# Kernel tuning notes

Hardware: AMD Instinct MI355X
Metric: run time of the kernel (lower is better)

## Reference

```python
import jax, jax.numpy as jnp
import numpy as np

NEG_SLOPE = 0.2

def _gat_layer(x, src, dst, W, a_src, a_dst, b, n_nodes):
    # x: [N, Fin], W: [Fin, Fout], a_src/a_dst: [Fout], b: [Fout]
    h = x @ W                                  # [N, Fout]
    alpha_s = h @ a_src                        # [N]
    alpha_d = h @ a_dst                        # [N]
    e = jax.nn.leaky_relu(alpha_s[src] + alpha_d[dst], NEG_SLOPE)  # [E]
    # softmax over edges grouped by destination node
    m = jax.ops.segment_max(e, dst, num_segments=n_nodes)
    ex = jnp.exp(e - m[dst])
    denom = jax.ops.segment_sum(ex, dst, num_segments=n_nodes)
    alpha = ex / denom[dst]                    # [E]
    out = jax.ops.segment_sum(h[src] * alpha[:, None], dst, num_segments=n_nodes)
    return out + b


def setup_inputs() -> dict:
    key = jax.random.key(0)
    N, E, INP = 50000, 1600000, 128
    topo = [32, 64, 128, 128]
    OUT = 16
    ks = jax.random.split(key, 32)
    inp = {}
    inp['x'] = jax.random.normal(ks[0], (N, INP), dtype=jnp.float32)
    inp['edge_index'] = jax.random.randint(ks[1], (2, E), 0, N, dtype=jnp.int64)
    dims = [INP] + topo
    ki = 2
    for i in range(4):
        fin, fout = dims[i], dims[i + 1]
        s = 1.0 / np.sqrt(fin)
        inp[f'W{i}'] = jax.random.normal(ks[ki], (fin, fout), dtype=jnp.float32) * s; ki += 1
        inp[f'a_src{i}'] = jax.random.normal(ks[ki], (fout,), dtype=jnp.float32) * (1.0 / np.sqrt(fout)); ki += 1
        inp[f'a_dst{i}'] = jax.random.normal(ks[ki], (fout,), dtype=jnp.float32) * (1.0 / np.sqrt(fout)); ki += 1
        inp[f'b{i}'] = jnp.zeros((fout,), dtype=jnp.float32); ki += 1
    inp['fc_W'] = jax.random.normal(ks[ki], (topo[-1], OUT), dtype=jnp.float32) * (1.0 / np.sqrt(topo[-1])); ki += 1
    inp['fc_b'] = jnp.zeros((OUT,), dtype=jnp.float32)
    return inp


def reference(x, edge_index, W0, a_src0, a_dst0, b0, W1, a_src1, a_dst1, b1,
              W2, a_src2, a_dst2, b2, W3, a_src3, a_dst3, b3, fc_W, fc_b):
    n = x.shape[0]
    loops = jnp.arange(n, dtype=edge_index.dtype)
    src = jnp.concatenate([edge_index[0], loops])  # add self-loops (GATConv default)
    dst = jnp.concatenate([edge_index[1], loops])
    layers = [(W0, a_src0, a_dst0, b0), (W1, a_src1, a_dst1, b1),
              (W2, a_src2, a_dst2, b2), (W3, a_src3, a_dst3, b3)]
    for (W, a_s, a_d, b) in layers:
        x = jax.nn.relu(_gat_layer(x, src, dst, W, a_s, a_d, b, n))
    return x @ fc_W + fc_b
```

## Files before the change

kernel.cpp:

```cpp
#include <hip/hip_runtime.h>
#include <hip/hip_bf16.h>
#include <hip/hip_fp16.h>


__device__ __forceinline__ float bf2f(unsigned short w) {
    return __uint_as_float(((unsigned int)w) << 16);
}
__device__ __forceinline__ unsigned enc_f(float f) {
    unsigned u = __float_as_uint(f);
    return (u & 0x80000000u) ? ~u : (u | 0x80000000u);
}
__device__ __forceinline__ float dec_f(unsigned u) {
    unsigned v = (u & 0x80000000u) ? (u & 0x7FFFFFFFu) : ~u;
    return __uint_as_float(v);
}

#define ELL_K 96
#define NCHUNK 256

__global__ void detect_kernel(const unsigned short* __restrict__ xw,
                              const int* __restrict__ ew,
                              int* __restrict__ flags,
                              unsigned* __restrict__ maxbuf)
{
    __shared__ int cnt_sane[256];
    __shared__ int cnt_nz[256];
    const int t = threadIdx.x;
    unsigned short w = xw[2 * t];
    int e = (w >> 7) & 0xff;
    cnt_sane[t] = (e >= 110 && e <= 133) ? 1 : 0;
    cnt_nz[t] = (ew[2 * t + 1] != 0) ? 1 : 0;
    if (t < 8) maxbuf[t] = 0u;
    __syncthreads();
    if (t == 0) {
        int s = 0, nz = 0;
        for (int i = 0; i < 256; ++i) { s += cnt_sane[i]; nz += cnt_nz[i]; }
        flags[0] = (s >= 128) ? 1 : 0;
        flags[1] = (nz == 0) ? 1 : 0;
    }
}

struct ParamPtrs {
    const void* src[18];
    int n[18];
    int off[18];
};

__global__ void convert_params_kernel(ParamPtrs pp, const int* __restrict__ flags,
                                      float* __restrict__ out)
{
    const int b = blockIdx.x;
    const int n = pp.n[b];
    const float* fp = (const float*)pp.src[b];
    const unsigned short* hp = (const unsigned short*)pp.src[b];
    const int bf = flags[0];
    float* o = out + pp.off[b];
    for (int i = threadIdx.x; i < n; i += blockDim.x)
        o[i] = bf ? bf2f(hp[i]) : fp[i];
}

__global__ void wvec_kernel(const float* __restrict__ W1, const float* __restrict__ as1,
                            const float* __restrict__ ad1,
                            const float* __restrict__ W2, const float* __restrict__ as2,
                            const float* __restrict__ ad2,
                            float* __restrict__ wsd)
{
    const int l = blockIdx.x;
    const float* W  = l ? W2  : W1;
    const float* As = l ? as2 : as1;
    const float* Ad = l ? ad2 : ad1;
    const int FIN  = l ? 64 : 32;
    const int FOUT = l ? 128 : 64;
    float* ws = wsd + l * 256;
    float* wd = ws + 128;
    const int k = threadIdx.x;
    if (k < FIN) {
        float s = 0.f, d = 0.f;
        for (int j = 0; j < FOUT; ++j) {
            const float w = W[k * FOUT + j];
            s += w * As[j];
            d += w * Ad[j];
        }
        ws[k] = s;
        wd[k] = d;
    }
}

__global__ __launch_bounds__(256) void max_finalize_kernel(
    const float2* __restrict__ bm, int nb, unsigned* __restrict__ maxSD)
{
    __shared__ float sm[4][2];
    const int tx = threadIdx.x;
    float ms = -INFINITY, md = -INFINITY;
    for (int i = tx; i < nb; i += 256) {
        const float2 v = bm[i];
        ms = fmaxf(ms, v.x);
        md = fmaxf(md, v.y);
    }
    #pragma unroll
    for (int off = 32; off > 0; off >>= 1) {
        ms = fmaxf(ms, __shfl_down(ms, off, 64));
        md = fmaxf(md, __shfl_down(md, off, 64));
    }
    if ((tx & 63) == 0) { sm[tx >> 6][0] = ms; sm[tx >> 6][1] = md; }
    __syncthreads();
    if (tx == 0) {
        #pragma unroll
        for (int w = 1; w < 4; ++w) {
            ms = fmaxf(ms, sm[w][0]);
            md = fmaxf(md, sm[w][1]);
        }
        maxSD[0] = enc_f(ms);
        maxSD[1] = enc_f(md);
    }
}

template <int FIN>
__global__ __launch_bounds__(256) void alpha_matvec_kernel(
    const __half* __restrict__ x, const float* __restrict__ ws,
    const float* __restrict__ wd, float* __restrict__ as, float* __restrict__ ad,
    float2* __restrict__ blkmax, int N)
{
    constexpr int LPR = FIN / 8;
    constexpr int RPB = 256 / LPR;
    const int tx = threadIdx.x;
    const int lane = tx & 63;
    const long long row = (long long)blockIdx.x * RPB + tx / LPR;
    const int fl = (tx % LPR) * 8;
    float ss = 0.f, sd = 0.f;
    const bool valid = row < (long long)N;
    if (valid) {
        const float4 raw = *(const float4*)(x + row * FIN + fl);
        const __half2* q = (const __half2*)&raw;
        float v[8];
        float2 f;
        f = __half22float2(q[0]); v[0] = f.x; v[1] = f.y;
        f = __half22float2(q[1]); v[2] = f.x; v[3] = f.y;
        f = __half22float2(q[2]); v[4] = f.x; v[5] = f.y;
        f = __half22float2(q[3]); v[6] = f.x; v[7] = f.y;
        #pragma unroll
        for (int u = 0; u < 8; ++u) {
            const float r = fmaxf(v[u], 0.f);
            ss += r * ws[fl + u];
            sd += r * wd[fl + u];
        }
    }
    #pragma unroll
    for (int off = LPR / 2; off > 0; off >>= 1) {
        ss += __shfl_down(ss, off, 64);
        sd += __shfl_down(sd, off, 64);
    }
    const bool lead = (tx % LPR) == 0;
    if (lead && valid) { as[row] = ss; ad[row] = sd; }
    float ms = (lead && valid) ? ss : -INFINITY;
    float md = (lead && valid) ? sd : -INFINITY;
    #pragma unroll
    for (int off = 32; off > 0; off >>= 1) {
        ms = fmaxf(ms, __shfl_down(ms, off, 64));
        md = fmaxf(md, __shfl_down(md, off, 64));
    }
    if (lane == 0)
        blkmax[blockIdx.x * 4 + (tx >> 6)] = make_float2(ms, md);
}

__global__ __launch_bounds__(1024) void hist_pack_kernel(
    const int* __restrict__ e, const int* __restrict__ flags,
    unsigned* __restrict__ sd, unsigned* __restrict__ hist,
    long long E, long long Et, int chunk, int NQ)
{
    extern __shared__ unsigned hcnt[];
    const int c = blockIdx.x;
    for (int i = threadIdx.x; i < NQ; i += 1024) hcnt[i] = 0u;
    __syncthreads();
    const int f64 = flags[1];
    const long long c0 = (long long)c * chunk;
    long long c1 = c0 + chunk; if (c1 > Et) c1 = Et;
    for (long long t = c0 + threadIdx.x; t < c1; t += 1024) {
        int s, d;
        if (t >= E) { s = (int)(t - E); d = s; }
        else if (f64) { s = e[2 * t]; d = e[2 * E + 2 * t]; }
        else          { s = e[t];     d = e[E + t]; }
        sd[t] = (unsigned)s | ((unsigned)d << 16);
        atomicAdd(&hcnt[d >> 2], 1u << ((d & 3) << 3));
    }
    __syncthreads();
    unsigned* hrow = hist + (size_t)c * NQ;
    for (int i = threadIdx.x; i < NQ; i += 1024) hrow[i] = hcnt[i];
}

__global__ __launch_bounds__(256) void chunk_scan_kernel(
    const unsigned* __restrict__ hist, unsigned* __restrict__ base32,
    int* __restrict__ deg, int NQ, int N)
{
    __shared__ unsigned short sums[32][8][4];
    const int dql = threadIdx.x & 31;
    const int oct = threadIdx.x >> 5;
    const int dq  = blockIdx.x * 32 + dql;
    const int cbeg = oct * 32;

    unsigned s0 = 0, s1 = 0, s2 = 0, s3 = 0;
    if (dq < NQ) {
        const unsigned* hp = hist + (size_t)cbeg * NQ + dq;
        #pragma unroll 8
        for (int c = 0; c < 32; ++c) {
            const unsigned v = hp[(size_t)c * NQ];
            s0 += v & 0xffu;          s1 += (v >> 8) & 0xffu;
            s2 += (v >> 16) & 0xffu;  s3 += v >> 24;
        }
    }
    sums[dql][oct][0] = (unsigned short)s0;
    sums[dql][oct][1] = (unsigned short)s1;
    sums[dql][oct][2] = (unsigned short)s2;
    sums[dql][oct][3] = (unsigned short)s3;
    __syncthreads();

    unsigned r0 = 0, r1 = 0, r2 = 0, r3 = 0;
    #pragma unroll
    for (int p = 0; p < 8; ++p) {
        if (p < oct) {
            r0 += sums[dql][p][0]; r1 += sums[dql][p][1];
            r2 += sums[dql][p][2]; r3 += sums[dql][p][3];
        }
    }
    if (dq >= NQ) return;

    if (oct == 7) {
        const int d0 = dq * 4;
        const int t0 = (int)(r0 + s0), t1 = (int)(r1 + s1);
        const int t2 = (int)(r2 + s2), t3 = (int)(r3 + s3);
        if (d0 + 3 < N) {
            *(int4*)(deg + d0) = make_int4(t0, t1, t2, t3);
        } else {
            if (d0     < N) deg[d0]     = t0;
            if (d0 + 1 < N) deg[d0 + 1] = t1;
            if (d0 + 2 < N) deg[d0 + 2] = t2;
            if (d0 + 3 < N) deg[d0 + 3] = t3;
        }
    }

    unsigned run0 = r0, run1 = r1, run2 = r2, run3 = r3;
    const unsigned* hp = hist + (size_t)cbeg * NQ + dq;
    unsigned* bp = base32 + (size_t)cbeg * NQ + dq;
    for (int c = 0; c < 32; ++c) {
        const unsigned v = hp[(size_t)c * NQ];
        const unsigned o = (run0 < 255u ? run0 : 255u)
                         | ((run1 < 255u ? run1 : 255u) << 8)
                         | ((run2 < 255u ? run2 : 255u) << 16)
                         | ((run3 < 255u ? run3 : 255u) << 24);
        bp[(size_t)c * NQ] = o;
        run0 += v & 0xffu;          run1 += (v >> 8) & 0xffu;
        run2 += (v >> 16) & 0xffu;  run3 += v >> 24;
    }
}

__global__ __launch_bounds__(256) void ell_fill_kernel(
    const unsigned* __restrict__ sd, const unsigned* __restrict__ base32,
    unsigned short* __restrict__ ell16, long long Et, int chunk, int NQ, int shift)
{
    extern __shared__ unsigned cnt[];
    const int bucket = blockIdx.x & 7;
    const int c = blockIdx.x >> 3;
    const int words = (1 << shift) >> 2;
    for (int i = threadIdx.x; i < words; i += 256) cnt[i] = 0u;
    __syncthreads();
    const long long c0 = (long long)c * chunk;
    long long c1 = c0 + chunk; if (c1 > Et) c1 = Et;
    const unsigned* brow = base32 + (size_t)c * NQ;
    const int dlo = bucket << shift;
    for (long long i = c0 + threadIdx.x; i < c1; i += 256) {
        const unsigned v = sd[i];
        const int d = (int)(v >> 16);
        if ((d >> shift) != bucket) continue;
        const int dl = d - dlo;
        const unsigned sh = (unsigned)((dl & 3) << 3);
        const unsigned old = atomicAdd(&cnt[dl >> 2], 1u << sh);
        const unsigned lr = (old >> sh) & 0xffu;
        const unsigned b = (brow[d >> 2] >> ((d & 3) << 3)) & 0xffu;
        const unsigned slot = b + lr;
        if (slot < ELL_K)
            ell16[(long long)d * ELL_K + slot] = (unsigned short)(v & 0xffffu);
    }
}

struct Half4 { __half2 a, b; };

__device__ __forceinline__ void store4(float* h, long long idx, const float* a) {
    *(float4*)(h + idx) = make_float4(a[0], a[1], a[2], a[3]);
}
__device__ __forceinline__ void store4(__half* h, long long idx, const float* a) {
    Half4 v;
    v.a = __floats2half2_rn(a[0], a[1]);
    v.b = __floats2half2_rn(a[2], a[3]);
    *(Half4*)(h + idx) = v;
}

template <int FIN, int FOUT, typename OT>
__global__ __launch_bounds__(256) void gemm_alpha_kernel(
    const void* __restrict__ xv, const int* __restrict__ flags, int x_ext,
    const float* __restrict__ W, const float* __restrict__ a_src,
    const float* __restrict__ a_dst, const float* __restrict__ bias,
    OT* __restrict__ h,
    float* __restrict__ alpha_s, float* __restrict__ alpha_d,
    float2* __restrict__ blkmax, int has_alpha,
    int N, int relu_in, int has_bias)
{
    constexpr int CG = FOUT / 4;
    constexpr int RT = 256 / CG;
    constexpr int RR = 64 / RT;
    constexpr int TM = 64;
    constexpr int XP = FIN + 4;
    constexpr int Q  = FIN / 8;

    __shared__ float xs[TM * XP];
    __shared__ float red[2][TM][CG + 1];

    const int tx = threadIdx.x;
    const int cg = tx & (CG - 1);
    const int rt = tx / CG;
    const long long base = (long long)blockIdx.x * TM;

    const int xbf = x_ext ? flags[0] : 0;

    for (int idx = tx; idx < TM * Q; idx += 256) {
        const int r  = idx / Q;
        const int c8 = idx - r * Q;
        const long long grow = base + r;
        float v[8] = {0.f, 0.f, 0.f, 0.f, 0.f, 0.f, 0.f, 0.f};
        if (grow < N) {
            const long long gi = grow * FIN + 8 * c8;
            if (x_ext) {
                if (xbf) {
                    const unsigned short* xp = (const unsigned short*)xv + gi;
                    #pragma unroll
                    for (int u = 0; u < 8; ++u) v[u] = bf2f(xp[u]);
                } else {
                    const float4 f0 = *((const float4*)((const float*)xv + gi));
                    const float4 f1 = *((const float4*)((const float*)xv + gi + 4));
                    v[0] = f0.x; v[1] = f0.y; v[2] = f0.z; v[3] = f0.w;
                    v[4] = f1.x; v[5] = f1.y; v[6] = f1.z; v[7] = f1.w;
                }
            } else {
                const float4 raw = *((const float4*)((const __half*)xv + gi));
                const __half2* q = (const __half2*)&raw;
                const float2 a0 = __half22float2(q[0]);
                const float2 a1 = __half22float2(q[1]);
                const float2 a2 = __half22float2(q[2]);
                const float2 a3 = __half22float2(q[3]);
                v[0] = a0.x; v[1] = a0.y; v[2] = a1.x; v[3] = a1.y;
                v[4] = a2.x; v[5] = a2.y; v[6] = a3.x; v[7] = a3.y;
            }
            if (relu_in) {
                #pragma unroll
                for (int u = 0; u < 8; ++u) v[u] = fmaxf(v[u], 0.f);
            }
        }
        *(float4*)&xs[r * XP + 8 * c8]     = make_float4(v[0], v[1], v[2], v[3]);
        *(float4*)&xs[r * XP + 8 * c8 + 4] = make_float4(v[4], v[5], v[6], v[7]);
    }
    __syncthreads();

    float acc[RR][4];
    #pragma unroll
    for (int rr = 0; rr < RR; ++rr)
        { acc[rr][0] = acc[rr][1] = acc[rr][2] = acc[rr][3] = 0.f; }

    const int r0 = rt * RR;
    #pragma unroll 4
    for (int k = 0; k < FIN; ++k) {
        const float4 w4 = *(const float4*)(W + k * FOUT + 4 * cg);
        #pragma unroll
        for (int rr = 0; rr < RR; ++rr) {
            const float xval = xs[(r0 + rr) * XP + k];
            acc[rr][0] += xval * w4.x;
            acc[rr][1] += xval * w4.y;
            acc[rr][2] += xval * w4.z;
            acc[rr][3] += xval * w4.w;
        }
    }

    if (has_bias) {
        const float4 b4 = *(const float4*)(bias + 4 * cg);
        #pragma unroll
        for (int rr = 0; rr < RR; ++rr) {
            acc[rr][0] += b4.x; acc[rr][1] += b4.y;
            acc[rr][2] += b4.z; acc[rr][3] += b4.w;
        }
    }

    #pragma unroll
    for (int rr = 0; rr < RR; ++rr) {
        const long long grow = base + r0 + rr;
        if (grow < N)
            store4(h, grow * FOUT + 4 * cg, acc[rr]);
    }

    if (has_alpha) {
        const float4 as4 = *(const float4*)(a_src + 4 * cg);
        const float4 ad4 = *(const float4*)(a_dst + 4 * cg);
        #pragma unroll
        for (int rr = 0; rr < RR; ++rr) {
            red[0][r0 + rr][cg] = acc[rr][0] * as4.x + acc[rr][1] * as4.y
                                + acc[rr][2] * as4.z + acc[rr][3] * as4.w;
            red[1][r0 + rr][cg] = acc[rr][0] * ad4.x + acc[rr][1] * ad4.y
                                + acc[rr][2] * ad4.z + acc[rr][3] * ad4.w;
        }
        __syncthreads();
        if (tx < TM) {
            float ss = 0.f, sd = 0.f;
            #pragma unroll
            for (int j = 0; j < CG; ++j) {
                ss += red[0][tx][j];
                sd += red[1][tx][j];
            }
            const long long grow = base + tx;
            const bool valid = grow < N;
            if (valid) { alpha_s[grow] = ss; alpha_d[grow] = sd; }
            float ms = valid ? ss : -INFINITY;
            float md = valid ? sd : -INFINITY;
            #pragma unroll
            for (int off = 32; off > 0; off >>= 1) {
                ms = fmaxf(ms, __shfl_down(ms, off, 64));
                md = fmaxf(md, __shfl_down(md, off, 64));
            }
            if (tx == 0)
                blkmax[blockIdx.x] = make_float2(ms, md);
        }
    }
}

template <int F, int XRELU, int ADDB>
__global__ __launch_bounds__(256) void gat_gather_kernel(
    const int* __restrict__ deg, const unsigned short* __restrict__ ell16,
    const float* __restrict__ as, const float* __restrict__ ad,
    const unsigned* __restrict__ maxSD,
    const __half* __restrict__ h, const float* __restrict__ bias,
    __half* __restrict__ out, int N)
{
    constexpr int LPE = F / 8;
    constexpr int EPJ = 64 / LPE;

    const int wslot = threadIdx.x >> 6;
    const int lane = threadIdx.x & 63;
    const int d = blockIdx.x * 4 + wslot;
    if (d >= N) return;

    const float M = dec_f(maxSD[0]) + dec_f(maxSD[1]);
    const int cnt_all = min(deg[d], ELL_K);
    const long long e0 = (long long)d * ELL_K;
    const float add = ad[d];

    const int sub = lane / LPE;
    const int fl  = (lane % LPE) * 8;

    float den = 0.f;
    float a0 = 0.f, a1 = 0.f, a2 = 0.f, a3 = 0.f;
    float a4 = 0.f, a5 = 0.f, a6 = 0.f, a7 = 0.f;
    for (int base = 0; base < cnt_all; base += 64) {
        const int e = base + lane;
        float p = 0.f;
        int s = 0;
        if (e < cnt_all) {
            s = (int)ell16[e0 + e];
            float v = as[s] + add;
            v = (v > 0.f) ? v : 0.2f * v;
            p = expf(v - M);
        }
        den += p;
        const int cnt = min(64, cnt_all - base);
        for (int j = 0; j < cnt; j += 4 * EPJ) {
            float pj[4];
            float4 hv[4];
            #pragma unroll
            for (int u = 0; u < 4; ++u) {
                const int jj = j + u * EPJ + sub;
                pj[u] = __shfl(p, jj, 64);
                const int sj = __shfl(s, jj, 64);
                hv[u] = *(const float4*)(h + (long long)sj * F + fl);
            }
            #pragma unroll
            for (int u = 0; u < 4; ++u) {
                const __half2* q = (const __half2*)&hv[u];
                float2 f0 = __half22float2(q[0]);
                float2 f1 = __half22float2(q[1]);
                float2 f2 = __half22float2(q[2]);
                float2 f3 = __half22float2(q[3]);
                if (XRELU) {
                    f0.x = fmaxf(f0.x, 0.f); f0.y = fmaxf(f0.y, 0.f);
                    f1.x = fmaxf(f1.x, 0.f); f1.y = fmaxf(f1.y, 0.f);
                    f2.x = fmaxf(f2.x, 0.f); f2.y = fmaxf(f2.y, 0.f);
                    f3.x = fmaxf(f3.x, 0.f); f3.y = fmaxf(f3.y, 0.f);
                }
                a0 += pj[u] * f0.x;  a1 += pj[u] * f0.y;
                a2 += pj[u] * f1.x;  a3 += pj[u] * f1.y;
                a4 += pj[u] * f2.x;  a5 += pj[u] * f2.y;
                a6 += pj[u] * f3.x;  a7 += pj[u] * f3.y;
            }
        }
    }
    #pragma unroll
    for (int off = 32; off > 0; off >>= 1)
        den += __shfl_down(den, off, 64);
    den = __shfl(den, 0, 64);
    const float inv = 1.f / den;

    #pragma unroll
    for (int off = 32; off >= LPE; off >>= 1) {
        a0 += __shfl_down(a0, off, 64);
        a1 += __shfl_down(a1, off, 64);
        a2 += __shfl_down(a2, off, 64);
        a3 += __shfl_down(a3, off, 64);
        a4 += __shfl_down(a4, off, 64);
        a5 += __shfl_down(a5, off, 64);
        a6 += __shfl_down(a6, off, 64);
        a7 += __shfl_down(a7, off, 64);
    }
    if (lane < LPE) {
        float4 pack;
        __half2* q = (__half2*)&pack;
        if (ADDB) {
            const float4 bA = *(const float4*)(bias + fl);
            const float4 bB = *(const float4*)(bias + fl + 4);
            q[0] = __floats2half2_rn(bA.x + a0 * inv, bA.y + a1 * inv);
            q[1] = __floats2half2_rn(bA.z + a2 * inv, bA.w + a3 * inv);
            q[2] = __floats2half2_rn(bB.x + a4 * inv, bB.y + a5 * inv);
            q[3] = __floats2half2_rn(bB.z + a6 * inv, bB.w + a7 * inv);
        } else {
            q[0] = __floats2half2_rn(a0 * inv, a1 * inv);
            q[1] = __floats2half2_rn(a2 * inv, a3 * inv);
            q[2] = __floats2half2_rn(a4 * inv, a5 * inv);
            q[3] = __floats2half2_rn(a6 * inv, a7 * inv);
        }
        *(float4*)(out + (long long)d * F + fl) = pack;
    }
}

extern "C" void kernel_launch(void* const* d_in, const int* in_sizes, int n_in,
                              void* d_out, int out_size, void* d_ws, size_t ws_size,
                              hipStream_t stream)
{
    const int INP = 128;
    const int N = in_sizes[0] / INP;
    const long long E = in_sizes[1] / 2;
    const long long Et = E + N;

    const int Fin[4]  = {128, 32, 64, 128};
    const int Fout[4] = {32, 64, 128, 128};

    const int NQ = (N + 3) / 4;
    const size_t histBytes = (size_t)NQ * 4 * NCHUNK;
    const size_t xbufBytes = (size_t)N * 128 * sizeof(__half);
    const size_t bigBytes  = histBytes > xbufBytes ? histBytes : xbufBytes;

    char* p = (char*)d_ws;
    auto alloc = [&](size_t bytes) {
        char* r = p;
        p += (bytes + 255) & ~(size_t)255;
        return r;
    };
    __half*   bufH    = (__half*)  alloc(bigBytes);
    __half*   bufX    = (__half*)  alloc(bigBytes);
    float*    as      = (float*)   alloc((size_t)N * sizeof(float));
    float*    ad      = (float*)   alloc((size_t)N * sizeof(float));
    int*      deg     = (int*)     alloc((size_t)N * sizeof(int));
    unsigned short* ell16 = (unsigned short*)alloc((size_t)N * ELL_K * sizeof(unsigned short));
    unsigned* sd      = (unsigned*)alloc((size_t)Et * sizeof(unsigned));
    unsigned* maxbuf  = (unsigned*)alloc(64);
    int*      flags   = (int*)     alloc(64);
    float*    wsd     = (float*)   alloc(512 * sizeof(float));
    float2*   blkmax  = (float2*)  alloc(8192 * sizeof(float2));
    float*    params  = (float*)   alloc(64 * 1024 * sizeof(float));
    (void)ws_size;

    unsigned* hist   = (unsigned*)bufH;
    unsigned* base32 = (unsigned*)bufX;

    detect_kernel<<<1, 256, 0, stream>>>((const unsigned short*)d_in[0],
                                         (const int*)d_in[1], flags, maxbuf);

    ParamPtrs pp;
    int off = 0;
    {
        int k = 0;
        for (int i = 0; i < 4; ++i) {
            pp.n[k++] = Fin[i] * Fout[i];
            pp.n[k++] = Fout[i];
            pp.n[k++] = Fout[i];
            pp.n[k++] = Fout[i];
        }
        pp.n[16] = 128 * 16;
        pp.n[17] = 16;
        for (int i = 0; i < 18; ++i) {
            pp.src[i] = d_in[2 + i];
            pp.off[i] = off;
            off += pp.n[i];
        }
    }
    convert_params_kernel<<<18, 256, 0, stream>>>(pp, flags, params);

    const float* Wl[4], *asr[4], *adt[4], *bl[4];
    for (int i = 0; i < 4; ++i) {
        Wl[i]  = params + pp.off[4 * i + 0];
        asr[i] = params + pp.off[4 * i + 1];
        adt[i] = params + pp.off[4 * i + 2];
        bl[i]  = params + pp.off[4 * i + 3];
    }
    const float* fcW = params + pp.off[16];
    const float* fcb = params + pp.off[17];

    wvec_kernel<<<2, 128, 0, stream>>>(Wl[1], asr[1], adt[1],
                                       Wl[2], asr[2], adt[2], wsd);

    const int* e32 = (const int*)d_in[1];

    {
        const int chunk = (int)((Et + NCHUNK - 1) / NCHUNK);
        int shift = 0;
        while ((N >> shift) > 8) shift++;
        hist_pack_kernel<<<NCHUNK, 1024, (size_t)NQ * 4, stream>>>(
            e32, flags, sd, hist, E, Et, chunk, NQ);
        chunk_scan_kernel<<<(NQ + 31) / 32, 256, 0, stream>>>(
            hist, base32, deg, NQ, N);
        ell_fill_kernel<<<NCHUNK * 8, 256, (size_t)(1 << shift), stream>>>(
            sd, base32, ell16, Et, chunk, NQ, shift);
    }

    const int gblocks = (N + 3) / 4;
    const int mblocks = (N + 63) / 64;
    const void* xin = d_in[0];

    gemm_alpha_kernel<128, 32, __half><<<mblocks, 256, 0, stream>>>(
        xin, flags, 1, Wl[0], asr[0], adt[0], nullptr, bufH, as, ad,
        blkmax, 1, N, 0, 0);
    max_finalize_kernel<<<1, 256, 0, stream>>>(blkmax, mblocks, maxbuf + 0);
    gat_gather_kernel<32, 0, 1><<<gblocks, 256, 0, stream>>>(
        deg, ell16, as, ad, maxbuf + 0, bufH, bl[0], bufX, N);

    {
        const int ab = (N + 63) / 64;
        alpha_matvec_kernel<32><<<ab, 256, 0, stream>>>(
            bufX, wsd + 0, wsd + 128, as, ad, blkmax, N);
        max_finalize_kernel<<<1, 256, 0, stream>>>(blkmax, ab * 4, maxbuf + 2);
    }
    gat_gather_kernel<32, 1, 0><<<gblocks, 256, 0, stream>>>(
        deg, ell16, as, ad, maxbuf + 2, bufX, nullptr, bufH, N);
    gemm_alpha_kernel<32, 64, __half><<<mblocks, 256, 0, stream>>>(
        bufH, flags, 0, Wl[1], nullptr, nullptr, bl[1], bufX, nullptr, nullptr,
        nullptr, 0, N, 0, 1);

    {
        const int ab = (N + 31) / 32;
        alpha_matvec_kernel<64><<<ab, 256, 0, stream>>>(
            bufX, wsd + 256, wsd + 384, as, ad, blkmax, N);
        max_finalize_kernel<<<1, 256, 0, stream>>>(blkmax, ab * 4, maxbuf + 4);
    }
    gat_gather_kernel<64, 1, 0><<<gblocks, 256, 0, stream>>>(
        deg, ell16, as, ad, maxbuf + 4, bufX, nullptr, bufH, N);
    gemm_alpha_kernel<64, 128, __half><<<mblocks, 256, 0, stream>>>(
        bufH, flags, 0, Wl[2], nullptr, nullptr, bl[2], bufX, nullptr, nullptr,
        nullptr, 0, N, 0, 1);

    gemm_alpha_kernel<128, 128, __half><<<mblocks, 256, 0, stream>>>(
        bufX, flags, 0, Wl[3], asr[3], adt[3], nullptr, bufH, as, ad,
        blkmax, 1, N, 1, 0);
    max_finalize_kernel<<<1, 256, 0, stream>>>(blkmax, mblocks, maxbuf + 6);
    gat_gather_kernel<128, 0, 1><<<gblocks, 256, 0, stream>>>(
        deg, ell16, as, ad, maxbuf + 6, bufH, bl[3], bufX, N);

    gemm_alpha_kernel<128, 16, float><<<mblocks, 256, 0, stream>>>(
        bufX, flags, 0, fcW, nullptr, nullptr, fcb,
        (float*)d_out, nullptr, nullptr, nullptr, 0, N, 1, 1);
}
```

Before: 460.3 us.

## Fuse attention-logit matvecs into gather and GEMM epilogues, drop standalone kernels

Removes the separate alpha_matvec kernels. Layer-2 attention logits are now computed in the epilogue of the layer-1 gather, written to new as2/ad2 buffers along with per-block maxima. Layer-3 logits come from the layer-2 GEMM epilogue with a ReLU applied before the dot product. The wvec precompute is merged into the parameter-conversion kernel, reading raw inputs directly. This saves a full re-read of the hidden features and several launches, at the cost of a syncthreads and shared-memory reduction in every gather block.

```diff
diff --git a/kernel.cpp b/kernel.cpp
--- a/kernel.cpp
+++ b/kernel.cpp
@@ -47,28 +47,27 @@
 };
 
 __global__ void convert_params_kernel(ParamPtrs pp, const int* __restrict__ flags,
-                                      float* __restrict__ out)
+                                      float* __restrict__ out, float* __restrict__ wsd)
 {
     const int b = blockIdx.x;
-    const int n = pp.n[b];
-    const float* fp = (const float*)pp.src[b];
-    const unsigned short* hp = (const unsigned short*)pp.src[b];
     const int bf = flags[0];
-    float* o = out + pp.off[b];
-    for (int i = threadIdx.x; i < n; i += blockDim.x)
-        o[i] = bf ? bf2f(hp[i]) : fp[i];
-}
-
-__global__ void wvec_kernel(const float* __restrict__ W1, const float* __restrict__ as1,
-                            const float* __restrict__ ad1,
-                            const float* __restrict__ W2, const float* __restrict__ as2,
-                            const float* __restrict__ ad2,
-                            float* __restrict__ wsd)
-{
-    const int l = blockIdx.x;
-    const float* W  = l ? W2  : W1;
-    const float* As = l ? as2 : as1;
-    const float* Ad = l ? ad2 : ad1;
+    if (b < 18) {
+        const int n = pp.n[b];
+        const float* fp = (const float*)pp.src[b];
+        const unsigned short* hp = (const unsigned short*)pp.src[b];
+        float* o = out + pp.off[b];
+        for (int i = threadIdx.x; i < n; i += blockDim.x)
+            o[i] = bf ? bf2f(hp[i]) : fp[i];
+        return;
+    }
+    const int l = b - 18;
+    const int wi = l ? 8 : 4;
+    const unsigned short* Wh  = (const unsigned short*)pp.src[wi];
+    const float*          Wf  = (const float*)pp.src[wi];
+    const unsigned short* Ash = (const unsigned short*)pp.src[wi + 1];
+    const float*          Asf = (const float*)pp.src[wi + 1];
+    const unsigned short* Adh = (const unsigned short*)pp.src[wi + 2];
+    const float*          Adf = (const float*)pp.src[wi + 2];
     const int FIN  = l ? 64 : 32;
     const int FOUT = l ? 128 : 64;
     float* ws = wsd + l * 256;
@@ -77,9 +76,11 @@
     if (k < FIN) {
         float s = 0.f, d = 0.f;
         for (int j = 0; j < FOUT; ++j) {
-            const float w = W[k * FOUT + j];
-            s += w * As[j];
-            d += w * Ad[j];
+            const float w = bf ? bf2f(Wh[k * FOUT + j]) : Wf[k * FOUT + j];
+            const float a = bf ? bf2f(Ash[j]) : Asf[j];
+            const float c = bf ? bf2f(Adh[j]) : Adf[j];
+            s += w * a;
+            d += w * c;
         }
         ws[k] = s;
         wd[k] = d;
@@ -113,54 +114,6 @@
         maxSD[0] = enc_f(ms);
         maxSD[1] = enc_f(md);
     }
-}
-
-template <int FIN>
-__global__ __launch_bounds__(256) void alpha_matvec_kernel(
-    const __half* __restrict__ x, const float* __restrict__ ws,
-    const float* __restrict__ wd, float* __restrict__ as, float* __restrict__ ad,
-    float2* __restrict__ blkmax, int N)
-{
-    constexpr int LPR = FIN / 8;
-    constexpr int RPB = 256 / LPR;
-    const int tx = threadIdx.x;
-    const int lane = tx & 63;
-    const long long row = (long long)blockIdx.x * RPB + tx / LPR;
-    const int fl = (tx % LPR) * 8;
-    float ss = 0.f, sd = 0.f;
-    const bool valid = row < (long long)N;
-    if (valid) {
-        const float4 raw = *(const float4*)(x + row * FIN + fl);
-        const __half2* q = (const __half2*)&raw;
-        float v[8];
-        float2 f;
-        f = __half22float2(q[0]); v[0] = f.x; v[1] = f.y;
-        f = __half22float2(q[1]); v[2] = f.x; v[3] = f.y;
-        f = __half22float2(q[2]); v[4] = f.x; v[5] = f.y;
-        f = __half22float2(q[3]); v[6] = f.x; v[7] = f.y;
-        #pragma unroll
-        for (int u = 0; u < 8; ++u) {
-            const float r = fmaxf(v[u], 0.f);
-            ss += r * ws[fl + u];
-            sd += r * wd[fl + u];
-        }
-    }
-    #pragma unroll
-    for (int off = LPR / 2; off > 0; off >>= 1) {
-        ss += __shfl_down(ss, off, 64);
-        sd += __shfl_down(sd, off, 64);
-    }
-    const bool lead = (tx % LPR) == 0;
-    if (lead && valid) { as[row] = ss; ad[row] = sd; }
-    float ms = (lead && valid) ? ss : -INFINITY;
-    float md = (lead && valid) ? sd : -INFINITY;
-    #pragma unroll
-    for (int off = 32; off > 0; off >>= 1) {
-        ms = fmaxf(ms, __shfl_down(ms, off, 64));
-        md = fmaxf(md, __shfl_down(md, off, 64));
-    }
-    if (lane == 0)
-        blkmax[blockIdx.x * 4 + (tx >> 6)] = make_float2(ms, md);
 }
 
 __global__ __launch_bounds__(1024) void hist_pack_kernel(
@@ -302,7 +255,7 @@
     OT* __restrict__ h,
     float* __restrict__ alpha_s, float* __restrict__ alpha_d,
     float2* __restrict__ blkmax, int has_alpha,
-    int N, int relu_in, int has_bias)
+    int N, int relu_in, int has_bias, int relu_alpha)
 {
     constexpr int CG = FOUT / 4;
     constexpr int RT = 256 / CG;
@@ -399,10 +352,13 @@
         const float4 ad4 = *(const float4*)(a_dst + 4 * cg);
         #pragma unroll
         for (int rr = 0; rr < RR; ++rr) {
-            red[0][r0 + rr][cg] = acc[rr][0] * as4.x + acc[rr][1] * as4.y
-                                + acc[rr][2] * as4.z + acc[rr][3] * as4.w;
-            red[1][r0 + rr][cg] = acc[rr][0] * ad4.x + acc[rr][1] * ad4.y
-                                + acc[rr][2] * ad4.z + acc[rr][3] * ad4.w;
+            float b0 = acc[rr][0], b1 = acc[rr][1], b2 = acc[rr][2], b3 = acc[rr][3];
+            if (relu_alpha) {
+                b0 = fmaxf(b0, 0.f); b1 = fmaxf(b1, 0.f);
+                b2 = fmaxf(b2, 0.f); b3 = fmaxf(b3, 0.f);
+            }
+            red[0][r0 + rr][cg] = b0 * as4.x + b1 * as4.y + b2 * as4.z + b3 * as4.w;
+            red[1][r0 + rr][cg] = b0 * ad4.x + b1 * ad4.y + b2 * ad4.z + b3 * ad4.w;
         }
         __syncthreads();
         if (tx < TM) {
@@ -428,13 +384,16 @@
     }
 }
 
-template <int F, int XRELU, int ADDB>
+template <int F, int XRELU, int ADDB, int AFUSE>
 __global__ __launch_bounds__(256) void gat_gather_kernel(
     const int* __restrict__ deg, const unsigned short* __restrict__ ell16,
     const float* __restrict__ as, const float* __restrict__ ad,
     const unsigned* __restrict__ maxSD,
     const __half* __restrict__ h, const float* __restrict__ bias,
-    __half* __restrict__ out, int N)
+    __half* __restrict__ out, int N,
+    const float* __restrict__ wsA, const float* __restrict__ wdA,
+    float* __restrict__ asO, float* __restrict__ adO,
+    float2* __restrict__ bmax)
 {
     constexpr int LPE = F / 8;
     constexpr int EPJ = 64 / LPE;
@@ -442,95 +401,147 @@
     const int wslot = threadIdx.x >> 6;
     const int lane = threadIdx.x & 63;
     const int d = blockIdx.x * 4 + wslot;
-    if (d >= N) return;
-
-    const float M = dec_f(maxSD[0]) + dec_f(maxSD[1]);
-    const int cnt_all = min(deg[d], ELL_K);
-    const long long e0 = (long long)d * ELL_K;
-    const float add = ad[d];
-
-    const int sub = lane / LPE;
-    const int fl  = (lane % LPE) * 8;
-
-    float den = 0.f;
-    float a0 = 0.f, a1 = 0.f, a2 = 0.f, a3 = 0.f;
-    float a4 = 0.f, a5 = 0.f, a6 = 0.f, a7 = 0.f;
-    for (int base = 0; base < cnt_all; base += 64) {
-        const int e = base + lane;
-        float p = 0.f;
-        int s = 0;
-        if (e < cnt_all) {
-            s = (int)ell16[e0 + e];
-            float v = as[s] + add;
-            v = (v > 0.f) ? v : 0.2f * v;
-            p = expf(v - M);
-        }
-        den += p;
-        const int cnt = min(64, cnt_all - base);
-        for (int j = 0; j < cnt; j += 4 * EPJ) {
-            float pj[4];
-            float4 hv[4];
+    const bool dvalid = d < N;
+    if (!AFUSE && !dvalid) return;
+
+    float ssA = -INFINITY, sdA = -INFINITY;
+
+    if (dvalid) {
+        const float M = dec_f(maxSD[0]) + dec_f(maxSD[1]);
+        const int cnt_all = min(deg[d], ELL_K);
+        const long long e0 = (long long)d * ELL_K;
+        const float add = ad[d];
+
+        const int sub = lane / LPE;
+        const int fl  = (lane % LPE) * 8;
+
+        float den = 0.f;
+        float a0 = 0.f, a1 = 0.f, a2 = 0.f, a3 = 0.f;
+        float a4 = 0.f, a5 = 0.f, a6 = 0.f, a7 = 0.f;
+        for (int base = 0; base < cnt_all; base += 64) {
+            const int e = base + lane;
+            float p = 0.f;
+            int s = 0;
+            if (e < cnt_all) {
+                s = (int)ell16[e0 + e];
+                float v = as[s] + add;
+                v = (v > 0.f) ? v : 0.2f * v;
+                p = expf(v - M);
+            }
+            den += p;
+            const int cnt = min(64, cnt_all - base);
+            for (int j = 0; j < cnt; j += 4 * EPJ) {
+                float pj[4];
+                float4 hv[4];
+                #pragma unroll
+                for (int u = 0; u < 4; ++u) {
+                    const int jj = j + u * EPJ + sub;
+                    pj[u] = __shfl(p, jj, 64);
+                    const int sj = __shfl(s, jj, 64);
+                    hv[u] = *(const float4*)(h + (long long)sj * F + fl);
+                }
+                #pragma unroll
+                for (int u = 0; u < 4; ++u) {
+                    const __half2* q = (const __half2*)&hv[u];
+                    float2 f0 = __half22float2(q[0]);
+                    float2 f1 = __half22float2(q[1]);
+                    float2 f2 = __half22float2(q[2]);
+                    float2 f3 = __half22float2(q[3]);
+                    if (XRELU) {
+                        f0.x = fmaxf(f0.x, 0.f); f0.y = fmaxf(f0.y, 0.f);
+                        f1.x = fmaxf(f1.x, 0.f); f1.y = fmaxf(f1.y, 0.f);
+                        f2.x = fmaxf(f2.x, 0.f); f2.y = fmaxf(f2.y, 0.f);
+                        f3.x = fmaxf(f3.x, 0.f); f3.y = fmaxf(f3.y, 0.f);
+                    }
+                    a0 += pj[u] * f0.x;  a1 += pj[u] * f0.y;
+                    a2 += pj[u] * f1.x;  a3 += pj[u] * f1.y;
+                    a4 += pj[u] * f2.x;  a5 += pj[u] * f2.y;
+                    a6 += pj[u] * f3.x;  a7 += pj[u] * f3.y;
+                }
+            }
+        }
+        #pragma unroll
+        for (int off = 32; off > 0; off >>= 1)
+            den += __shfl_down(den, off, 64);
+        den = __shfl(den, 0, 64);
+        const float inv = 1.f / den;
+
+        #pragma unroll
+        for (int off = 32; off >= LPE; off >>= 1) {
+            a0 += __shfl_down(a0, off, 64);
+            a1 += __shfl_down(a1, off, 64);
+            a2 += __shfl_down(a2, off, 64);
+            a3 += __shfl_down(a3, off, 64);
+            a4 += __shfl_down(a4, off, 64);
+            a5 += __shfl_down(a5, off, 64);
+            a6 += __shfl_down(a6, off, 64);
+            a7 += __shfl_down(a7, off, 64);
+        }
+        if (lane < LPE) {
+            float v0, v1, v2, v3, v4, v5, v6, v7;
+            if (ADDB) {
+                const float4 bA = *(const float4*)(bias + fl);
+                const float4 bB = *(const float4*)(bias + fl + 4);
+                v0 = bA.x + a0 * inv;  v1 = bA.y + a1 * inv;
+                v2 = bA.z + a2 * inv;  v3 = bA.w + a3 * inv;
+                v4 = bB.x + a4 * inv;  v5 = bB.y + a5 * inv;
+                v6 = bB.z + a6 * inv;  v7 = bB.w + a7 * inv;
+            } else {
+                v0 = a0 * inv;  v1 = a1 * inv;  v2 = a2 * inv;  v3 = a3 * inv;
+                v4 = a4 * inv;  v5 = a5 * inv;  v6 = a6 * inv;  v7 = a7 * inv;
+            }
+            float4 pack;
+            __half2* q = (__half2*)&pack;
+            q[0] = __floats2half2_rn(v0, v1);
+            q[1] = __floats2half2_rn(v2, v3);
+            q[2] = __floats2half2_rn(v4, v5);
+            q[3] = __floats2half2_rn(v6, v7);
+            *(float4*)(out + (long long)d * F + fl) = pack;
+
+            if (AFUSE) {
+                const float4 wA = *(const float4*)(wsA + fl);
+                const float4 wB = *(const float4*)(wsA + fl + 4);
+                const float4 dA = *(const float4*)(wdA + fl);
+                const float4 dB = *(const float4*)(wdA + fl + 4);
+                const float r0 = fmaxf(v0, 0.f), r1 = fmaxf(v1, 0.f);
+                const float r2 = fmaxf(v2, 0.f), r3 = fmaxf(v3, 0.f);
+                const float r4 = fmaxf(v4, 0.f), r5 = fmaxf(v5, 0.f);
+                const float r6 = fmaxf(v6, 0.f), r7 = fmaxf(v7, 0.f);
+                float ss = r0 * wA.x + r1 * wA.y + r2 * wA.z + r3 * wA.w
+                         + r4 * wB.x + r5 * wB.y + r6 * wB.z + r7 * wB.w;
+                float sd = r0 * dA.x + r1 * dA.y + r2 * dA.z + r3 * dA.w
+                         + r4 * dB.x + r5 * dB.y + r6 * dB.z + r7 * dB.w;
+                #pragma unroll
+                for (int off = LPE / 2; off > 0; off >>= 1) {
+                    ss += __shfl_down(ss, off, 64);
+                    sd += __shfl_down(sd, off, 64);
+                }
+                if (lane == 0) {
+                    asO[d] = ss;
+                    adO[d] = sd;
+                    ssA = ss;
+                    sdA = sd;
+                }
+            }
+        }
+    }
+
+    if (AFUSE) {
+        __shared__ float smx[4][2];
+        if (lane == 0) {
+            smx[wslot][0] = dvalid ? ssA : -INFINITY;
+            smx[wslot][1] = dvalid ? sdA : -INFINITY;
+        }
+        __syncthreads();
+        if (threadIdx.x == 0) {
+            float ms = smx[0][0], md = smx[0][1];
             #pragma unroll
-            for (int u = 0; u < 4; ++u) {
-                const int jj = j + u * EPJ + sub;
-                pj[u] = __shfl(p, jj, 64);
-                const int sj = __shfl(s, jj, 64);
-                hv[u] = *(const float4*)(h + (long long)sj * F + fl);
-            }
-            #pragma unroll
-            for (int u = 0; u < 4; ++u) {
-                const __half2* q = (const __half2*)&hv[u];
-                float2 f0 = __half22float2(q[0]);
-                float2 f1 = __half22float2(q[1]);
-                float2 f2 = __half22float2(q[2]);
-                float2 f3 = __half22float2(q[3]);
-                if (XRELU) {
-                    f0.x = fmaxf(f0.x, 0.f); f0.y = fmaxf(f0.y, 0.f);
-                    f1.x = fmaxf(f1.x, 0.f); f1.y = fmaxf(f1.y, 0.f);
-                    f2.x = fmaxf(f2.x, 0.f); f2.y = fmaxf(f2.y, 0.f);
-                    f3.x = fmaxf(f3.x, 0.f); f3.y = fmaxf(f3.y, 0.f);
-                }
-                a0 += pj[u] * f0.x;  a1 += pj[u] * f0.y;
-                a2 += pj[u] * f1.x;  a3 += pj[u] * f1.y;
-                a4 += pj[u] * f2.x;  a5 += pj[u] * f2.y;
-                a6 += pj[u] * f3.x;  a7 += pj[u] * f3.y;
-            }
-        }
-    }
-    #pragma unroll
-    for (int off = 32; off > 0; off >>= 1)
-        den += __shfl_down(den, off, 64);
-    den = __shfl(den, 0, 64);
-    const float inv = 1.f / den;
-
-    #pragma unroll
-    for (int off = 32; off >= LPE; off >>= 1) {
-        a0 += __shfl_down(a0, off, 64);
-        a1 += __shfl_down(a1, off, 64);
-        a2 += __shfl_down(a2, off, 64);
-        a3 += __shfl_down(a3, off, 64);
-        a4 += __shfl_down(a4, off, 64);
-        a5 += __shfl_down(a5, off, 64);
-        a6 += __shfl_down(a6, off, 64);
-        a7 += __shfl_down(a7, off, 64);
-    }
-    if (lane < LPE) {
-        float4 pack;
-        __half2* q = (__half2*)&pack;
-        if (ADDB) {
-            const float4 bA = *(const float4*)(bias + fl);
-            const float4 bB = *(const float4*)(bias + fl + 4);
-            q[0] = __floats2half2_rn(bA.x + a0 * inv, bA.y + a1 * inv);
-            q[1] = __floats2half2_rn(bA.z + a2 * inv, bA.w + a3 * inv);
-            q[2] = __floats2half2_rn(bB.x + a4 * inv, bB.y + a5 * inv);
-            q[3] = __floats2half2_rn(bB.z + a6 * inv, bB.w + a7 * inv);
-        } else {
-            q[0] = __floats2half2_rn(a0 * inv, a1 * inv);
-            q[1] = __floats2half2_rn(a2 * inv, a3 * inv);
-            q[2] = __floats2half2_rn(a4 * inv, a5 * inv);
-            q[3] = __floats2half2_rn(a6 * inv, a7 * inv);
-        }
-        *(float4*)(out + (long long)d * F + fl) = pack;
+            for (int w = 1; w < 4; ++w) {
+                ms = fmaxf(ms, smx[w][0]);
+                md = fmaxf(md, smx[w][1]);
+            }
+            bmax[blockIdx.x] = make_float2(ms, md);
+        }
     }
 }
 
@@ -561,13 +572,15 @@
     __half*   bufX    = (__half*)  alloc(bigBytes);
     float*    as      = (float*)   alloc((size_t)N * sizeof(float));
     float*    ad      = (float*)   alloc((size_t)N * sizeof(float));
+    float*    as2     = (float*)   alloc((size_t)N * sizeof(float));
+    float*    ad2     = (float*)   alloc((size_t)N * sizeof(float));
     int*      deg     = (int*)     alloc((size_t)N * sizeof(int));
     unsigned short* ell16 = (unsigned short*)alloc((size_t)N * ELL_K * sizeof(unsigned short));
     unsigned* sd      = (unsigned*)alloc((size_t)Et * sizeof(unsigned));
     unsigned* maxbuf  = (unsigned*)alloc(64);
     int*      flags   = (int*)     alloc(64);
     float*    wsd     = (float*)   alloc(512 * sizeof(float));
-    float2*   blkmax  = (float2*)  alloc(8192 * sizeof(float2));
+    float2*   blkmax  = (float2*)  alloc(16384 * sizeof(float2));
     float*    params  = (float*)   alloc(64 * 1024 * sizeof(float));
     (void)ws_size;
 
@@ -595,7 +608,7 @@
             off += pp.n[i];
         }
     }
-    convert_params_kernel<<<18, 256, 0, stream>>>(pp, flags, params);
+    convert_params_kernel<<<20, 256, 0, stream>>>(pp, flags, params, wsd);
 
     const float* Wl[4], *asr[4], *adt[4], *bl[4];
     for (int i = 0; i < 4; ++i) {
@@ -606,9 +619,6 @@
     }
     const float* fcW = params + pp.off[16];
     const float* fcb = params + pp.off[17];
-
-    wvec_kernel<<<2, 128, 0, stream>>>(Wl[1], asr[1], adt[1],
-                                       Wl[2], asr[2], adt[2], wsd);
 
     const int* e32 = (const int*)d_in[1];
 
@@ -630,43 +640,37 @@
 
     gemm_alpha_kernel<128, 32, __half><<<mblocks, 256, 0, stream>>>(
         xin, flags, 1, Wl[0], asr[0], adt[0], nullptr, bufH, as, ad,
-        blkmax, 1, N, 0, 0);
+        blkmax, 1, N, 0, 0, 0);
     max_finalize_kernel<<<1, 256, 0, stream>>>(blkmax, mblocks, maxbuf + 0);
-    gat_gather_kernel<32, 0, 1><<<gblocks, 256, 0, stream>>>(
-        deg, ell16, as, ad, maxbuf + 0, bufH, bl[0], bufX, N);
-
-    {
-        const int ab = (N + 63) / 64;
-        alpha_matvec_kernel<32><<<ab, 256, 0, stream>>>(
-            bufX, wsd + 0, wsd + 128, as, ad, blkmax, N);
-        max_finalize_kernel<<<1, 256, 0, stream>>>(blkmax, ab * 4, maxbuf + 2);
-    }
-    gat_gather_kernel<32, 1, 0><<<gblocks, 256, 0, stream>>>(
-        deg, ell16, as, ad, maxbuf + 2, bufX, nullptr, bufH, N);
+    gat_gather_kernel<32, 0, 1, 1><<<gblocks, 256, 0, stream>>>(
+        deg, ell16, as, ad, maxbuf + 0, bufH, bl[0], bufX, N,
+        wsd + 0, wsd + 128, as2, ad2, blkmax);
+    max_finalize_kernel<<<1, 256, 0, stream>>>(blkmax, gblocks, maxbuf + 2);
+
+    gat_gather_kernel<32, 1, 0, 0><<<gblocks, 256, 0, stream>>>(
+        deg, ell16, as2, ad2, maxbuf + 2, bufX, nullptr, bufH, N,
+        nullptr, nullptr, nullptr, nullptr, nullptr);
     gemm_alpha_kernel<32, 64, __half><<<mblocks, 256, 0, stream>>>(
-        bufH, flags, 0, Wl[1], nullptr, nullptr, bl[1], bufX, nullptr, nullptr,
-        nullptr, 0, N, 0, 1);
-
-    {
-        const int ab = (N + 31) / 32;
-        alpha_matvec_kernel<64><<<ab, 256, 0, stream>>>(
-            bufX, wsd + 256, wsd + 384, as, ad, blkmax, N);
-        max_finalize_kernel<<<1, 256, 0, stream>>>(blkmax, ab * 4, maxbuf + 4);
-    }
-    gat_gather_kernel<64, 1, 0><<<gblocks, 256, 0, stream>>>(
-        deg, ell16, as, ad, maxbuf + 4, bufX, nullptr, bufH, N);
+        bufH, flags, 0, Wl[1], wsd + 256, wsd + 384, bl[1], bufX, as, ad,
+        blkmax, 1, N, 0, 1, 1);
+    max_finalize_kernel<<<1, 256, 0, stream>>>(blkmax, mblocks, maxbuf + 4);
+
+    gat_gather_kernel<64, 1, 0, 0><<<gblocks, 256, 0, stream>>>(
+        deg, ell16, as, ad, maxbuf + 4, bufX, nullptr, bufH, N,
+        nullptr, nullptr, nullptr, nullptr, nullptr);
     gemm_alpha_kernel<64, 128, __half><<<mblocks, 256, 0, stream>>>(
         bufH, flags, 0, Wl[2], nullptr, nullptr, bl[2], bufX, nullptr, nullptr,
-        nullptr, 0, N, 0, 1);
+        nullptr, 0, N, 0, 1, 0);
 
     gemm_alpha_kernel<128, 128, __half><<<mblocks, 256, 0, stream>>>(
         bufX, flags, 0, Wl[3], asr[3], adt[3], nullptr, bufH, as, ad,
-        blkmax, 1, N, 1, 0);
+        blkmax, 1, N, 1, 0, 0);
     max_finalize_kernel<<<1, 256, 0, stream>>>(blkmax, mblocks, maxbuf + 6);
-    gat_gather_kernel<128, 0, 1><<<gblocks, 256, 0, stream>>>(
-        deg, ell16, as, ad, maxbuf + 6, bufH, bl[3], bufX, N);
+    gat_gather_kernel<128, 0, 1, 0><<<gblocks, 256, 0, stream>>>(
+        deg, ell16, as, ad, maxbuf + 6, bufH, bl[3], bufX, N,
+        nullptr, nullptr, nullptr, nullptr, nullptr);
 
     gemm_alpha_kernel<128, 16, float><<<mblocks, 256, 0, stream>>>(
         bufX, flags, 0, fcW, nullptr, nullptr, fcb,
-        (float*)d_out, nullptr, nullptr, nullptr, 0, N, 1, 1);
-}
+        (float*)d_out, nullptr, nullptr, nullptr, 0, N, 1, 1, 0);
+}
```

Measured after the change: 456.2 us (median of 2 runs). No clear change (-0.9%).
